# Kernel optimization log

Hardware: AMD Instinct MI355X
Metric: run time of the kernel (lower is better)

Reference implementation:

```python
import jax, jax.numpy as jnp
import numpy as np

N_NODES = 100000


def gcn_conv(x, W, src, dst, n):
    """PyG GCNConv with bias=False: add self-loops, symmetric norm, scatter-add."""
    h = x @ W  # [N, out]
    # degree including self-loop (all edge weights = 1)
    deg = jnp.zeros((n,), dtype=x.dtype).at[dst].add(1.0) + 1.0
    inv_sqrt = jax.lax.rsqrt(deg)  # deg >= 1 so safe
    edge_norm = inv_sqrt[src] * inv_sqrt[dst]  # [E]
    # neighbor aggregation: out_i = sum_{j->i} norm_ji * h_j
    agg = jnp.zeros_like(h).at[dst].add(h[src] * edge_norm[:, None])
    # self-loop contribution: norm_ii = 1/deg_i
    return agg + h * (inv_sqrt * inv_sqrt)[:, None]


def setup_inputs() -> dict:
    key = jax.random.key(0)
    k1, k2, k3, k4 = jax.random.split(key, 4)
    x = jax.random.normal(k1, (N_NODES, 128), dtype=jnp.float32)
    edge_index = jax.random.randint(k2, (2, 1600000), 0, N_NODES, dtype=jnp.int32)
    W1 = jax.random.normal(k3, (128, 64), dtype=jnp.float32) * (1.0 / np.sqrt(128))
    W2 = jax.random.normal(k4, (64, 40), dtype=jnp.float32) * (1.0 / np.sqrt(64))
    return {"x": x, "edge_index": edge_index, "W1": W1, "W2": W2}


def reference(x, edge_index, W1, W2):
    n = x.shape[0]
    src, dst = edge_index[0], edge_index[1]
    # layer 1 (dropout p=0.0 is identity) + relu
    h = jax.nn.relu(gcn_conv(x, W1, src, dst, n))
    # layer 2 + relu, then squeeze
    out = jax.nn.relu(gcn_conv(h, W2, src, dst, n))
    return jnp.squeeze(out)
```

## Files before the change

kernel.cpp:

```cpp
#include <hip/hip_runtime.h>
#include <hip/hip_fp16.h>


#define F0 128
#define F1 64
#define F2 40
#define H2S 64
#define ELLW 64
#define GEMM_BLKS 768
#define NRANK (GEMM_BLKS / 3)
#define STG_GM 512

__global__ void k_zero(int* __restrict__ cnt, int n) {
    const int i = blockIdx.x * blockDim.x + threadIdx.x;
    if (i < n) cnt[i] = 0;
}

__global__ __launch_bounds__(256) void k_gemmrank(const float* __restrict__ x,
                                                  const float* __restrict__ W,
                                                  __half* __restrict__ h,
                                                  const int* __restrict__ ei,
                                                  int* __restrict__ cnt,
                                                  int* __restrict__ ell,
                                                  int n, int E) {
    __shared__ float Wl[F0 * F1];
    __shared__ float xs[32 * F0];
    const int bid = blockIdx.x;
    const int tid = threadIdx.x;

    if ((bid % 3) == 2) {
        const int rb = bid / 3;
        const int stride = NRANK * 256;
#pragma unroll 4
        for (int e = rb * 256 + tid; e < E; e += stride) {
            const int s = ei[e];
            const int d = ei[E + e];
            const int r = atomicAdd(&cnt[d], 1);
            if (r < ELLW) ell[(long long)d * ELLW + r] = s;
        }
        return;
    }

    const int gid = bid - bid / 3;
    const int c = tid & 63;
    const int rq = tid >> 6;

    {
        float4* Wl4 = (float4*)Wl;
        const float4* Wg4 = (const float4*)W;
#pragma unroll
        for (int j = 0; j < (F0 * F1 / 4) / 256; ++j)
            Wl4[j * 256 + tid] = Wg4[j * 256 + tid];
    }
    __syncthreads();

    const int NG = GEMM_BLKS - NRANK;
    const int ntiles = (n + 31) >> 5;
    for (int tile = gid; tile < ntiles; tile += NG) {
        float4* xs4w = (float4*)xs;
#pragma unroll
        for (int j = 0; j < 4; ++j) {
            int fi = j * 256 + tid;
            int row = fi >> 5;
            int rg = tile * 32 + row;
            if (rg > n - 1) rg = n - 1;
            const float4* xrow = (const float4*)(x + (long long)rg * F0);
            xs4w[fi] = xrow[fi & 31];
        }
        __syncthreads();

        float acc[8] = {0.f,0.f,0.f,0.f,0.f,0.f,0.f,0.f};
#pragma unroll 2
        for (int b = 0; b < 32; ++b) {
            const float w0 = Wl[(4 * b + 0) * F1 + c];
            const float w1 = Wl[(4 * b + 1) * F1 + c];
            const float w2 = Wl[(4 * b + 2) * F1 + c];
            const float w3 = Wl[(4 * b + 3) * F1 + c];
#pragma unroll
            for (int i = 0; i < 8; ++i) {
                float4 xv = ((const float4*)xs)[(rq * 8 + i) * 32 + b];
                acc[i] = fmaf(xv.w, w3, fmaf(xv.z, w2, fmaf(xv.y, w1, fmaf(xv.x, w0, acc[i]))));
            }
        }

#pragma unroll
        for (int i = 0; i < 8; ++i) {
            int rg = tile * 32 + rq * 8 + i;
            if (rg < n) h[(long long)rg * F1 + c] = __float2half(acc[i]);
        }
        __syncthreads();
    }
}

__global__ void k_rsqrt_scale(const int* __restrict__ cnt, float* __restrict__ invs,
                              __half* __restrict__ h, int n, int gINV) {
    const int bid = blockIdx.x;
    const int tid = threadIdx.x;
    if (bid < gINV) {
        const int i = bid * 256 + tid;
        if (i < n) invs[i] = rsqrtf((float)(cnt[i] + 1));
    } else {
        const int fb = bid - gINV;
        const long long total4 = (long long)n * F1 / 4;
        long long i4 = (long long)fb * 256 + tid;
        const long long stride = (long long)2048 * 256;
        for (; i4 < total4; i4 += stride) {
            const int r = (int)(i4 >> 4);
            const float iv = rsqrtf((float)(cnt[r] + 1));
            __half2* hp = (__half2*)h + i4 * 2;
            __half2 a = hp[0], b = hp[1];
            float2 af = __half22float2(a), bf = __half22float2(b);
            af.x *= iv; af.y *= iv; bf.x *= iv; bf.y *= iv;
            hp[0] = __float22half2_rn(af);
            hp[1] = __float22half2_rn(bf);
        }
    }
}


__device__ __forceinline__ void gemm2_body(const __half* __restrict__ g,
                                           const float* __restrict__ W,
                                           const float* __restrict__ invs,
                                           __half* __restrict__ h,
                                           int n, int lo, int hi,
                                           int relbid, int nblk, int tid) {
    __shared__ float Wl[F1 * F2];
    __shared__ float xs[32 * F1];
    const int c = tid & 63;
    const int rq = tid >> 6;

    for (int i = tid; i < F1 * F2; i += 256) Wl[i] = W[i];
    __syncthreads();

    const int t0 = lo >> 5;
    const int ntiles = (hi - lo + 31) >> 5;
    for (int ti = relbid; ti < ntiles; ti += nblk) {
        const int tile = t0 + ti;
        {
            const int row = tid >> 3;
            const int ch  = tid & 7;
            int rg = tile * 32 + row;
            if (rg > n - 1) rg = n - 1;
            const float4 raw = *(const float4*)(g + (long long)rg * F1 + ch * 8);
            const __half2* hp = (const __half2*)&raw;
            const float2 f0 = __half22float2(hp[0]);
            const float2 f1 = __half22float2(hp[1]);
            const float2 f2 = __half22float2(hp[2]);
            const float2 f3 = __half22float2(hp[3]);
            float4* dst = (float4*)&xs[row * F1 + ch * 8];
            dst[0] = make_float4(f0.x, f0.y, f1.x, f1.y);
            dst[1] = make_float4(f2.x, f2.y, f3.x, f3.y);
        }
        __syncthreads();

        if (c < F2) {
            float acc[8] = {0.f,0.f,0.f,0.f,0.f,0.f,0.f,0.f};
#pragma unroll 2
            for (int b = 0; b < 16; ++b) {
                const float w0 = Wl[(4 * b + 0) * F2 + c];
                const float w1 = Wl[(4 * b + 1) * F2 + c];
                const float w2 = Wl[(4 * b + 2) * F2 + c];
                const float w3 = Wl[(4 * b + 3) * F2 + c];
#pragma unroll
                for (int i = 0; i < 8; ++i) {
                    float4 xv = ((const float4*)xs)[(rq * 8 + i) * 16 + b];
                    acc[i] = fmaf(xv.w, w3, fmaf(xv.z, w2, fmaf(xv.y, w1, fmaf(xv.x, w0, acc[i]))));
                }
            }
#pragma unroll
            for (int i = 0; i < 8; ++i) {
                int rg = tile * 32 + rq * 8 + i;
                if (rg < hi) h[(long long)rg * H2S + c] = __float2half(acc[i] * invs[rg]);
            }
        }
        __syncthreads();
    }
}

__device__ __forceinline__ void gather64_body(const int* __restrict__ cnt,
                                              const int* __restrict__ ell,
                                              const float* __restrict__ invs,
                                              const __half* __restrict__ h,
                                              __half* __restrict__ g,
                                              int lo, int hi, int relbid, int tid) {
    const int w = lo + relbid * 4 + (tid >> 6);
    const int lane = tid & 63;
    if (w >= hi) return;
    const int deg = min(cnt[w], ELLW);
    const int* row = ell + (long long)w * ELLW;
    float acc0 = 0.f, acc1 = 0.f, acc2 = 0.f, acc3 = 0.f;
    int k = 0;
    for (; k + 16 <= deg; k += 16) {
        int ss[16];
#pragma unroll
        for (int j = 0; j < 16; ++j) ss[j] = row[k + j];
        float vv[16];
#pragma unroll
        for (int j = 0; j < 16; ++j)
            vv[j] = __half2float(h[(long long)ss[j] * F1 + lane]);
        acc0 += ((vv[0] + vv[4]) + (vv[8]  + vv[12]));
        acc1 += ((vv[1] + vv[5]) + (vv[9]  + vv[13]));
        acc2 += ((vv[2] + vv[6]) + (vv[10] + vv[14]));
        acc3 += ((vv[3] + vv[7]) + (vv[11] + vv[15]));
    }
    for (; k + 8 <= deg; k += 8) {
        const int s0 = row[k+0], s1 = row[k+1], s2 = row[k+2], s3 = row[k+3];
        const int s4 = row[k+4], s5 = row[k+5], s6 = row[k+6], s7 = row[k+7];
        const float v0 = __half2float(h[(long long)s0 * F1 + lane]);
        const float v1 = __half2float(h[(long long)s1 * F1 + lane]);
        const float v2 = __half2float(h[(long long)s2 * F1 + lane]);
        const float v3 = __half2float(h[(long long)s3 * F1 + lane]);
        const float v4 = __half2float(h[(long long)s4 * F1 + lane]);
        const float v5 = __half2float(h[(long long)s5 * F1 + lane]);
        const float v6 = __half2float(h[(long long)s6 * F1 + lane]);
        const float v7 = __half2float(h[(long long)s7 * F1 + lane]);
        acc0 += v0 + v4; acc1 += v1 + v5; acc2 += v2 + v6; acc3 += v3 + v7;
    }
    for (; k + 2 <= deg; k += 2) {
        const int s0 = row[k], s1 = row[k+1];
        acc0 += __half2float(h[(long long)s0 * F1 + lane]);
        acc1 += __half2float(h[(long long)s1 * F1 + lane]);
    }
    if (k < deg) {
        acc0 += __half2float(h[(long long)row[k] * F1 + lane]);
    }
    const float iv = invs[w];
    const float self = __half2float(h[(long long)w * F1 + lane]);
    g[(long long)w * F1 + lane] =
        __float2half(fmaxf(iv * (((acc0 + acc1) + (acc2 + acc3)) + self), 0.f));
}


__global__ __launch_bounds__(256) void k_gather64(const int* __restrict__ cnt,
                                                  const int* __restrict__ ell,
                                                  const float* __restrict__ invs,
                                                  const __half* __restrict__ h,
                                                  __half* __restrict__ g,
                                                  int lo, int hi) {
    gather64_body(cnt, ell, invs, h, g, lo, hi, blockIdx.x, threadIdx.x);
}

__global__ __launch_bounds__(256, 8) void k_stage(const __half* __restrict__ g1,
                                                  const float* __restrict__ W2,
                                                  const float* __restrict__ invs,
                                                  __half* __restrict__ h2,
                                                  const int* __restrict__ cnt,
                                                  const int* __restrict__ ell,
                                                  const __half* __restrict__ h1,
                                                  __half* __restrict__ g1out,
                                                  int n,
                                                  int nGm, int gmlo, int gmhi,
                                                  int g64lo, int g64hi) {
    const int bid = blockIdx.x;
    const int tid = threadIdx.x;
    if (bid < nGm) {
        gemm2_body(g1, W2, invs, h2, n, gmlo, gmhi, bid, nGm, tid);
    } else {
        gather64_body(cnt, ell, invs, h1, g1out, g64lo, g64hi, bid - nGm, tid);
    }
}

__global__ __launch_bounds__(256) void k_gemm2(const __half* __restrict__ g,
                                               const float* __restrict__ W,
                                               const float* __restrict__ invs,
                                               __half* __restrict__ h,
                                               int n, int lo, int hi) {
    gemm2_body(g, W, invs, h, n, lo, hi, blockIdx.x, gridDim.x, threadIdx.x);
}

__global__ __launch_bounds__(256) void k_gather40(const int* __restrict__ cnt,
                                                  const int* __restrict__ ell,
                                                  const float* __restrict__ invs,
                                                  const __half* __restrict__ h,
                                                  float* __restrict__ g, int n) {
    const int w = (blockIdx.x * blockDim.x + threadIdx.x) >> 6;
    const int lane = threadIdx.x & 63;
    if (w >= n) return;
    const int deg = min(cnt[w], ELLW);
    const int* row = ell + (long long)w * ELLW;
    float acc0 = 0.f, acc1 = 0.f, acc2 = 0.f, acc3 = 0.f;
    int k = 0;
    if (lane < F2) {
        for (; k + 16 <= deg; k += 16) {
            int ss[16];
#pragma unroll
            for (int j = 0; j < 16; ++j) ss[j] = row[k + j];
            float vv[16];
#pragma unroll
            for (int j = 0; j < 16; ++j)
                vv[j] = __half2float(h[(long long)ss[j] * H2S + lane]);
            acc0 += ((vv[0] + vv[4]) + (vv[8]  + vv[12]));
            acc1 += ((vv[1] + vv[5]) + (vv[9]  + vv[13]));
            acc2 += ((vv[2] + vv[6]) + (vv[10] + vv[14]));
            acc3 += ((vv[3] + vv[7]) + (vv[11] + vv[15]));
        }
        for (; k + 8 <= deg; k += 8) {
            const int s0 = row[k+0], s1 = row[k+1], s2 = row[k+2], s3 = row[k+3];
            const int s4 = row[k+4], s5 = row[k+5], s6 = row[k+6], s7 = row[k+7];
            const float v0 = __half2float(h[(long long)s0 * H2S + lane]);
            const float v1 = __half2float(h[(long long)s1 * H2S + lane]);
            const float v2 = __half2float(h[(long long)s2 * H2S + lane]);
            const float v3 = __half2float(h[(long long)s3 * H2S + lane]);
            const float v4 = __half2float(h[(long long)s4 * H2S + lane]);
            const float v5 = __half2float(h[(long long)s5 * H2S + lane]);
            const float v6 = __half2float(h[(long long)s6 * H2S + lane]);
            const float v7 = __half2float(h[(long long)s7 * H2S + lane]);
            acc0 += v0 + v4; acc1 += v1 + v5; acc2 += v2 + v6; acc3 += v3 + v7;
        }
        for (; k + 2 <= deg; k += 2) {
            const int s0 = row[k], s1 = row[k+1];
            acc0 += __half2float(h[(long long)s0 * H2S + lane]);
            acc1 += __half2float(h[(long long)s1 * H2S + lane]);
        }
        if (k < deg) {
            acc0 += __half2float(h[(long long)row[k] * H2S + lane]);
        }
        const float iv = invs[w];
        const float self = __half2float(h[(long long)w * H2S + lane]);
        g[(long long)w * F2 + lane] = fmaxf(iv * (((acc0 + acc1) + (acc2 + acc3)) + self), 0.f);
    }
}

extern "C" void kernel_launch(void* const* d_in, const int* in_sizes, int n_in,
                              void* d_out, int out_size, void* d_ws, size_t ws_size,
                              hipStream_t stream) {
    const float* x  = (const float*)d_in[0];
    const int*   ei = (const int*)d_in[1];
    const float* W1 = (const float*)d_in[2];
    const float* W2 = (const float*)d_in[3];
    float* out = (float*)d_out;
    const int n = in_sizes[0] / F0;
    const int E = in_sizes[1] / 2;

    const size_t np = ((size_t)n + 65) & ~(size_t)63;
    char* wsb = (char*)d_ws;
    int*    cnt  = (int*)wsb;
    float*  invs = (float*)(cnt + np);
    int*    ell  = (int*)(invs + np);
    __half* h1h  = (__half*)(ell + (size_t)n * ELLW);
    __half* g1h  = h1h + (size_t)n * F1;
    __half* h2h  = g1h + (size_t)n * F1;

    const int nh = ((n / 2 + 31) / 32) * 32;
    const int gN = (n + 255) / 256;
    const int nA = (nh + 3) / 4;
    const int nB = (n - nh + 3) / 4;
    const int gW = (int)(((long long)n * 64 + 255) / 256);

    hipLaunchKernelGGL(k_zero, dim3(gN), dim3(256), 0, stream, cnt, n);
    hipLaunchKernelGGL(k_gemmrank, dim3(GEMM_BLKS), dim3(256), 0, stream,
                       x, W1, h1h, ei, cnt, ell, n, E);
    hipLaunchKernelGGL(k_rsqrt_scale, dim3(gN + 2048), dim3(256), 0, stream,
                       cnt, invs, h1h, n, gN);
    hipLaunchKernelGGL(k_gather64, dim3(nA), dim3(256), 0, stream,
                       cnt, ell, invs, h1h, g1h, 0, nh);
    hipLaunchKernelGGL(k_stage, dim3(STG_GM + nB), dim3(256), 0, stream,
                       g1h, W2, invs, h2h, cnt, ell, h1h, g1h,
                       n, STG_GM, 0, nh, nh, n);
    hipLaunchKernelGGL(k_gemm2, dim3(GEMM_BLKS), dim3(256), 0, stream,
                       g1h, W2, invs, h2h, n, nh, n);
    hipLaunchKernelGGL(k_gather40, dim3(gW), dim3(256), 0, stream,
                       cnt, ell, invs, h2h, out, n);
}
```

Before: 222.9 us.

## Fuse layer-1 gather with layer-2 GEMM per wavefront via shuffles

Replaces the split gather64 / staged gemm2 / gemm2 pipeline with a single persistent kernel. Each wavefront aggregates one node's 64 features and immediately multiplies by W2 using lane shuffles and a shared-memory copy of W2. The intermediate g1 buffer and its write/read round trip are removed, along with two launches. In exchange the GEMM becomes a serial 64-step shuffle+FMA loop per node, in which 24 of the 64 lanes do redundant work.

```diff
diff --git a/kernel.cpp b/kernel.cpp
--- a/kernel.cpp
+++ b/kernel.cpp
@@ -9,7 +9,6 @@
 #define ELLW 64
 #define GEMM_BLKS 768
 #define NRANK (GEMM_BLKS / 3)
-#define STG_GM 512
 
 __global__ void k_zero(int* __restrict__ cnt, int n) {
     const int i = blockIdx.x * blockDim.x + threadIdx.x;
@@ -117,155 +116,74 @@
     }
 }
 
-
-__device__ __forceinline__ void gemm2_body(const __half* __restrict__ g,
-                                           const float* __restrict__ W,
-                                           const float* __restrict__ invs,
-                                           __half* __restrict__ h,
-                                           int n, int lo, int hi,
-                                           int relbid, int nblk, int tid) {
+__global__ __launch_bounds__(256) void k_gathergemm2(const int* __restrict__ cnt,
+                                                     const int* __restrict__ ell,
+                                                     const float* __restrict__ invs,
+                                                     const __half* __restrict__ h1,
+                                                     const float* __restrict__ W2,
+                                                     __half* __restrict__ h2, int n) {
     __shared__ float Wl[F1 * F2];
-    __shared__ float xs[32 * F1];
-    const int c = tid & 63;
-    const int rq = tid >> 6;
-
-    for (int i = tid; i < F1 * F2; i += 256) Wl[i] = W[i];
+    const int tid = threadIdx.x;
+    for (int i = tid; i < F1 * F2; i += 256) Wl[i] = W2[i];
     __syncthreads();
 
-    const int t0 = lo >> 5;
-    const int ntiles = (hi - lo + 31) >> 5;
-    for (int ti = relbid; ti < ntiles; ti += nblk) {
-        const int tile = t0 + ti;
-        {
-            const int row = tid >> 3;
-            const int ch  = tid & 7;
-            int rg = tile * 32 + row;
-            if (rg > n - 1) rg = n - 1;
-            const float4 raw = *(const float4*)(g + (long long)rg * F1 + ch * 8);
-            const __half2* hp = (const __half2*)&raw;
-            const float2 f0 = __half22float2(hp[0]);
-            const float2 f1 = __half22float2(hp[1]);
-            const float2 f2 = __half22float2(hp[2]);
-            const float2 f3 = __half22float2(hp[3]);
-            float4* dst = (float4*)&xs[row * F1 + ch * 8];
-            dst[0] = make_float4(f0.x, f0.y, f1.x, f1.y);
-            dst[1] = make_float4(f2.x, f2.y, f3.x, f3.y);
-        }
-        __syncthreads();
-
-        if (c < F2) {
-            float acc[8] = {0.f,0.f,0.f,0.f,0.f,0.f,0.f,0.f};
-#pragma unroll 2
-            for (int b = 0; b < 16; ++b) {
-                const float w0 = Wl[(4 * b + 0) * F2 + c];
-                const float w1 = Wl[(4 * b + 1) * F2 + c];
-                const float w2 = Wl[(4 * b + 2) * F2 + c];
-                const float w3 = Wl[(4 * b + 3) * F2 + c];
-#pragma unroll
-                for (int i = 0; i < 8; ++i) {
-                    float4 xv = ((const float4*)xs)[(rq * 8 + i) * 16 + b];
-                    acc[i] = fmaf(xv.w, w3, fmaf(xv.z, w2, fmaf(xv.y, w1, fmaf(xv.x, w0, acc[i]))));
-                }
-            }
-#pragma unroll
-            for (int i = 0; i < 8; ++i) {
-                int rg = tile * 32 + rq * 8 + i;
-                if (rg < hi) h[(long long)rg * H2S + c] = __float2half(acc[i] * invs[rg]);
-            }
-        }
-        __syncthreads();
-    }
-}
-
-__device__ __forceinline__ void gather64_body(const int* __restrict__ cnt,
-                                              const int* __restrict__ ell,
-                                              const float* __restrict__ invs,
-                                              const __half* __restrict__ h,
-                                              __half* __restrict__ g,
-                                              int lo, int hi, int relbid, int tid) {
-    const int w = lo + relbid * 4 + (tid >> 6);
+    const int wv = tid >> 6;
     const int lane = tid & 63;
-    if (w >= hi) return;
-    const int deg = min(cnt[w], ELLW);
-    const int* row = ell + (long long)w * ELLW;
-    float acc0 = 0.f, acc1 = 0.f, acc2 = 0.f, acc3 = 0.f;
-    int k = 0;
-    for (; k + 16 <= deg; k += 16) {
-        int ss[16];
-#pragma unroll
-        for (int j = 0; j < 16; ++j) ss[j] = row[k + j];
-        float vv[16];
-#pragma unroll
-        for (int j = 0; j < 16; ++j)
-            vv[j] = __half2float(h[(long long)ss[j] * F1 + lane]);
-        acc0 += ((vv[0] + vv[4]) + (vv[8]  + vv[12]));
-        acc1 += ((vv[1] + vv[5]) + (vv[9]  + vv[13]));
-        acc2 += ((vv[2] + vv[6]) + (vv[10] + vv[14]));
-        acc3 += ((vv[3] + vv[7]) + (vv[11] + vv[15]));
-    }
-    for (; k + 8 <= deg; k += 8) {
-        const int s0 = row[k+0], s1 = row[k+1], s2 = row[k+2], s3 = row[k+3];
-        const int s4 = row[k+4], s5 = row[k+5], s6 = row[k+6], s7 = row[k+7];
-        const float v0 = __half2float(h[(long long)s0 * F1 + lane]);
-        const float v1 = __half2float(h[(long long)s1 * F1 + lane]);
-        const float v2 = __half2float(h[(long long)s2 * F1 + lane]);
-        const float v3 = __half2float(h[(long long)s3 * F1 + lane]);
-        const float v4 = __half2float(h[(long long)s4 * F1 + lane]);
-        const float v5 = __half2float(h[(long long)s5 * F1 + lane]);
-        const float v6 = __half2float(h[(long long)s6 * F1 + lane]);
-        const float v7 = __half2float(h[(long long)s7 * F1 + lane]);
-        acc0 += v0 + v4; acc1 += v1 + v5; acc2 += v2 + v6; acc3 += v3 + v7;
-    }
-    for (; k + 2 <= deg; k += 2) {
-        const int s0 = row[k], s1 = row[k+1];
-        acc0 += __half2float(h[(long long)s0 * F1 + lane]);
-        acc1 += __half2float(h[(long long)s1 * F1 + lane]);
-    }
-    if (k < deg) {
-        acc0 += __half2float(h[(long long)row[k] * F1 + lane]);
-    }
-    const float iv = invs[w];
-    const float self = __half2float(h[(long long)w * F1 + lane]);
-    g[(long long)w * F1 + lane] =
-        __float2half(fmaxf(iv * (((acc0 + acc1) + (acc2 + acc3)) + self), 0.f));
-}
-
-
-__global__ __launch_bounds__(256) void k_gather64(const int* __restrict__ cnt,
-                                                  const int* __restrict__ ell,
-                                                  const float* __restrict__ invs,
-                                                  const __half* __restrict__ h,
-                                                  __half* __restrict__ g,
-                                                  int lo, int hi) {
-    gather64_body(cnt, ell, invs, h, g, lo, hi, blockIdx.x, threadIdx.x);
-}
-
-__global__ __launch_bounds__(256, 8) void k_stage(const __half* __restrict__ g1,
-                                                  const float* __restrict__ W2,
-                                                  const float* __restrict__ invs,
-                                                  __half* __restrict__ h2,
-                                                  const int* __restrict__ cnt,
-                                                  const int* __restrict__ ell,
-                                                  const __half* __restrict__ h1,
-                                                  __half* __restrict__ g1out,
-                                                  int n,
-                                                  int nGm, int gmlo, int gmhi,
-                                                  int g64lo, int g64hi) {
-    const int bid = blockIdx.x;
-    const int tid = threadIdx.x;
-    if (bid < nGm) {
-        gemm2_body(g1, W2, invs, h2, n, gmlo, gmhi, bid, nGm, tid);
-    } else {
-        gather64_body(cnt, ell, invs, h1, g1out, g64lo, g64hi, bid - nGm, tid);
-    }
-}
-
-__global__ __launch_bounds__(256) void k_gemm2(const __half* __restrict__ g,
-                                               const float* __restrict__ W,
-                                               const float* __restrict__ invs,
-                                               __half* __restrict__ h,
-                                               int n, int lo, int hi) {
-    gemm2_body(g, W, invs, h, n, lo, hi, blockIdx.x, gridDim.x, threadIdx.x);
+    const int cc = (lane < F2) ? lane : (F2 - 1);
+    const int waves = gridDim.x * 4;
+
+    for (int w = blockIdx.x * 4 + wv; w < n; w += waves) {
+        const int deg = min(cnt[w], ELLW);
+        const int* row = ell + (long long)w * ELLW;
+        float acc0 = 0.f, acc1 = 0.f, acc2 = 0.f, acc3 = 0.f;
+        int k = 0;
+        for (; k + 16 <= deg; k += 16) {
+            int ss[16];
+#pragma unroll
+            for (int j = 0; j < 16; ++j) ss[j] = row[k + j];
+            float vv[16];
+#pragma unroll
+            for (int j = 0; j < 16; ++j)
+                vv[j] = __half2float(h1[(long long)ss[j] * F1 + lane]);
+            acc0 += ((vv[0] + vv[4]) + (vv[8]  + vv[12]));
+            acc1 += ((vv[1] + vv[5]) + (vv[9]  + vv[13]));
+            acc2 += ((vv[2] + vv[6]) + (vv[10] + vv[14]));
+            acc3 += ((vv[3] + vv[7]) + (vv[11] + vv[15]));
+        }
+        for (; k + 8 <= deg; k += 8) {
+            const int s0 = row[k+0], s1 = row[k+1], s2 = row[k+2], s3 = row[k+3];
+            const int s4 = row[k+4], s5 = row[k+5], s6 = row[k+6], s7 = row[k+7];
+            const float v0 = __half2float(h1[(long long)s0 * F1 + lane]);
+            const float v1 = __half2float(h1[(long long)s1 * F1 + lane]);
+            const float v2 = __half2float(h1[(long long)s2 * F1 + lane]);
+            const float v3 = __half2float(h1[(long long)s3 * F1 + lane]);
+            const float v4 = __half2float(h1[(long long)s4 * F1 + lane]);
+            const float v5 = __half2float(h1[(long long)s5 * F1 + lane]);
+            const float v6 = __half2float(h1[(long long)s6 * F1 + lane]);
+            const float v7 = __half2float(h1[(long long)s7 * F1 + lane]);
+            acc0 += v0 + v4; acc1 += v1 + v5; acc2 += v2 + v6; acc3 += v3 + v7;
+        }
+        for (; k + 2 <= deg; k += 2) {
+            const int s0 = row[k], s1 = row[k+1];
+            acc0 += __half2float(h1[(long long)s0 * F1 + lane]);
+            acc1 += __half2float(h1[(long long)s1 * F1 + lane]);
+        }
+        if (k < deg) {
+            acc0 += __half2float(h1[(long long)row[k] * F1 + lane]);
+        }
+        const float iv = invs[w];
+        const float self = __half2float(h1[(long long)w * F1 + lane]);
+        const float grow = fmaxf(iv * (((acc0 + acc1) + (acc2 + acc3)) + self), 0.f);
+
+        float o = 0.f;
+#pragma unroll 4
+        for (int kk = 0; kk < F1; ++kk) {
+            const float bc = __shfl(grow, kk, 64);
+            o = fmaf(bc, Wl[kk * F2 + cc], o);
+        }
+        if (lane < F2)
+            h2[(long long)w * H2S + lane] = __float2half(o * iv);
+    }
 }
 
 __global__ __launch_bounds__(256) void k_gather40(const int* __restrict__ cnt,
@@ -338,27 +256,19 @@
     float*  invs = (float*)(cnt + np);
     int*    ell  = (int*)(invs + np);
     __half* h1h  = (__half*)(ell + (size_t)n * ELLW);
-    __half* g1h  = h1h + (size_t)n * F1;
-    __half* h2h  = g1h + (size_t)n * F1;
-
-    const int nh = ((n / 2 + 31) / 32) * 32;
+    __half* h2h  = h1h + (size_t)n * F1;
+
     const int gN = (n + 255) / 256;
-    const int nA = (nh + 3) / 4;
-    const int nB = (n - nh + 3) / 4;
     const int gW = (int)(((long long)n * 64 + 255) / 256);
+    const int gGG = 2048;
 
     hipLaunchKernelGGL(k_zero, dim3(gN), dim3(256), 0, stream, cnt, n);
     hipLaunchKernelGGL(k_gemmrank, dim3(GEMM_BLKS), dim3(256), 0, stream,
                        x, W1, h1h, ei, cnt, ell, n, E);
     hipLaunchKernelGGL(k_rsqrt_scale, dim3(gN + 2048), dim3(256), 0, stream,
                        cnt, invs, h1h, n, gN);
-    hipLaunchKernelGGL(k_gather64, dim3(nA), dim3(256), 0, stream,
-                       cnt, ell, invs, h1h, g1h, 0, nh);
-    hipLaunchKernelGGL(k_stage, dim3(STG_GM + nB), dim3(256), 0, stream,
-                       g1h, W2, invs, h2h, cnt, ell, h1h, g1h,
-                       n, STG_GM, 0, nh, nh, n);
-    hipLaunchKernelGGL(k_gemm2, dim3(GEMM_BLKS), dim3(256), 0, stream,
-                       g1h, W2, invs, h2h, n, nh, n);
+    hipLaunchKernelGGL(k_gathergemm2, dim3(gGG), dim3(256), 0, stream,
+                       cnt, ell, invs, h1h, W2, h2h, n);
     hipLaunchKernelGGL(k_gather40, dim3(gW), dim3(256), 0, stream,
                        cnt, ell, invs, h2h, out, n);
 }
```

Result: slower. 258.5 us (+16.0%).
